# Optimization experiments

Measured on AMD Instinct MI355X. Metric: run time of the kernel, lower is better.

Reference implementation:

```python
import jax, jax.numpy as jnp
import numpy as np

# Forest of complete L-ary trees, BFS level-contiguous node numbering.
B_TREES, ARITY, DEPTH = 8, 4, 8
C, M, NGEN = 8, 100, 4
COUNTS = [B_TREES * ARITY**l for l in range(DEPTH + 1)]
OFFS = np.concatenate([[0], np.cumsum(COUNTS)]).astype(np.int64)
DIM = int(OFFS[-1])  # 699048
# tree id of each node: within-level index // (ARITY**level)
BATCH = np.concatenate([np.arange(COUNTS[l]) // (ARITY**l) for l in range(DEPTH + 1)])


def setup_inputs() -> dict:
    key = jax.random.key(0)
    k1, k2, k3, k4 = jax.random.split(key, 4)
    return {
        "x": jax.random.randint(k1, (DIM,), 0, M, dtype=jnp.int32),
        "A": jax.random.normal(k2, (C, C, ARITY, NGEN), dtype=jnp.float32) * 2.5,
        "B_emit": jax.random.normal(k3, (C, M, NGEN), dtype=jnp.float32) * 2.5,
        "Pi": jax.random.normal(k4, (C, NGEN), dtype=jnp.float32) * 2.5,
    }


def _htmm_loglik(x, A, B_emit, Pi):
    # softmax reparameterization (matches F.softmax axes in torch code)
    smA = jax.nn.softmax(A, axis=0)            # [C,C,L,G], over child state
    smA_t = jnp.transpose(smA, (2, 0, 1, 3))   # [L,C,C,G]
    smB = jax.nn.softmax(B_emit, axis=1)       # [C,M,G]
    smPi = jax.nn.softmax(Pi, axis=0)          # [C,G]

    # preliminary downward: prior state distribution per node, level by level.
    # Children of a parent are contiguous with sibling position j = idx % ARITY.
    prior_lvls = [jnp.broadcast_to(smPi, (COUNTS[0], C, NGEN))]
    for l in range(1, DEPTH + 1):
        n_pa = COUNTS[l - 1]
        # prior_child[c] = sum_d A[c, d, pos_j, g] * prior_pa[d]
        pl = jnp.einsum('jcdg,pdg->pjcg', smA_t, prior_lvls[-1])
        prior_lvls.append(pl.reshape(n_pa * ARITY, C, NGEN))
    prior = jnp.concatenate(prior_lvls, axis=0)  # [DIM,C,G]

    em = jnp.transpose(smB[:, x], (1, 0, 2))     # [DIM,C,G]
    beta0 = prior * em

    ll = jnp.zeros((DIM, NGEN), dtype=beta0.dtype)
    # leaves = deepest level
    beta_lvl = beta0[OFFS[DEPTH]:OFFS[DEPTH + 1]]
    nu = beta_lvl.sum(1)                          # [n_leaves,G]
    beta_lvl = beta_lvl / nu[:, None, :]
    ll = ll.at[OFFS[DEPTH]:OFFS[DEPTH + 1]].set(jnp.log(nu))

    # upward recursion, bottom-up
    for l in range(DEPTH, 0, -1):
        n_pa = COUNTS[l - 1]
        ratio = (beta_lvl / prior[OFFS[l]:OFFS[l + 1]]).reshape(n_pa, ARITY, C, NGEN)
        # beta_uv[d] = sum_c A[c, d, pos_j, g] * beta_ch[c] / prior_ch[c]
        beta_uv = jnp.einsum('jcdg,pjcg->pjdg', smA_t, ratio)  # [n_pa,L,C,G]
        beta_pa = beta0[OFFS[l - 1]:OFFS[l]] * jnp.prod(beta_uv, axis=1)
        nu = beta_pa.sum(1)
        beta_lvl = beta_pa / nu[:, None, :]
        ll = ll.at[OFFS[l - 1]:OFFS[l]].set(jnp.log(nu))

    # scatter per-node log-likelihood contributions into per-tree totals
    return jax.ops.segment_sum(ll, jnp.asarray(BATCH), num_segments=B_TREES)  # [B_TREES,G]


def reference(x, A, B_emit, Pi):
    return _htmm_loglik(x, A, B_emit, Pi)
```

## Files before the change

### kernel.cpp

```cpp
#include <hip/hip_runtime.h>

constexpr int OFFS1 = 8, OFFS2 = 40, OFFS3 = 168, OFFS4 = 680;
constexpr int OFFS5 = 2728, OFFS6 = 10920, OFFS7 = 43688, OFFS8 = 174760;


#define WB() __builtin_amdgcn_wave_barrier()
#define AG_ST(p, v) __hip_atomic_store((p), (v), __ATOMIC_RELAXED, __HIP_MEMORY_SCOPE_AGENT)
#define AG_LD(p) __hip_atomic_load((p), __ATOMIC_RELAXED, __HIP_MEMORY_SCOPE_AGENT)

template <int CTRL>
static __device__ __forceinline__ float qadd(float v) {
  int x = __builtin_amdgcn_update_dpp(0, __float_as_int(v), CTRL, 0xF, 0xF, true);
  return v + __int_as_float(x);
}
static __device__ __forceinline__ float bfly8(float v) {
  v = qadd<0xB1>(v);
  v = qadd<0x4E>(v);
  int x = __builtin_amdgcn_ds_swizzle(__float_as_int(v), 0x101F);
  return v + __int_as_float(x);
}

static __device__ __forceinline__ void ld8(const float* p, float pv[8]) {
  const float4* q = (const float4*)p;
  float4 a = q[0], b = q[1];
  pv[0] = a.x; pv[1] = a.y; pv[2] = a.z; pv[3] = a.w;
  pv[4] = b.x; pv[5] = b.y; pv[6] = b.z; pv[7] = b.w;
}

static __device__ __forceinline__ float dot8r(const float w[8], const float* p) {
  const float4* q = (const float4*)p;
  float4 a = q[0], b = q[1];
  return w[0] * a.x + w[1] * a.y + w[2] * a.z + w[3] * a.w +
         w[4] * b.x + w[5] * b.y + w[6] * b.z + w[7] * b.w;
}

static __device__ __forceinline__ float rcpf(float x) { return __builtin_amdgcn_rcpf(x); }

__global__ __launch_bounds__(256) void k_all(const int* __restrict__ x,
                                             const float* __restrict__ A,
                                             const float* __restrict__ Bm,
                                             const float* __restrict__ Pi,
                                             float* __restrict__ RAT4,
                                             float* __restrict__ blocksum,
                                             unsigned* __restrict__ ctr,
                                             float* __restrict__ out) {
  __shared__ __align__(16) float wtd_l[1024];
  __shared__ __align__(16) float emt_l[3200];
  __shared__ __align__(16) float pit_l[32];
  __shared__ __align__(16) float etab_l[12800];
  __shared__ __align__(16) float shbuf[2304];
  __shared__ __align__(16) float rat5buf[16][32];
  __shared__ __align__(16) float pri4buf[4][32];
  __shared__ float llb[4];
  __shared__ int lastf;

  int t = threadIdx.x;
  int r = t & 31, g = r >> 3, s = r & 7, grp = t >> 5;
  int b = blockIdx.x, tree = b >> 6;

  if (t < 128) {
    int d = t >> 4, j = (t >> 2) & 3, gg = t & 3;
    float v[8], sum = 0.f;
#pragma unroll
    for (int ss = 0; ss < 8; ss++) { v[ss] = __expf(A[((ss * 8 + d) * 4 + j) * 4 + gg]); sum += v[ss]; }
    float inv = rcpf(sum);
#pragma unroll
    for (int ss = 0; ss < 8; ss++) wtd_l[(j * 8 + d) * 32 + gg * 8 + ss] = v[ss] * inv;
  }
  if (t < 4) {
    float v[8], sum = 0.f;
#pragma unroll
    for (int c = 0; c < 8; c++) { v[c] = __expf(Pi[c * 4 + t]); sum += v[c]; }
    float inv = rcpf(sum);
#pragma unroll
    for (int c = 0; c < 8; c++) pit_l[t * 8 + c] = v[c] * inv;
    llb[t] = 0.f;
  }
  {
    int row = t >> 3, part = t & 7, c = row >> 2, gg = row & 3;
    int m0 = part < 4 ? part * 13 : 52 + (part - 4) * 12;
    int mn = part < 4 ? 13 : 12;
    float sum = 0.f;
    for (int m = m0; m < m0 + mn; m++) sum += __expf(Bm[(c * 100 + m) * 4 + gg]);
    sum = bfly8(sum);
    float inv = rcpf(sum);
    for (int m = m0; m < m0 + mn; m++)
      emt_l[m * 32 + gg * 8 + c] = __expf(Bm[(c * 100 + m) * 4 + gg]) * inv;
  }
  __syncthreads();
  {
    int c7 = t & 127, half = t >> 7;
    int j = c7 >> 5, d = (c7 >> 2) & 7, gg = c7 & 3;
    float w[8];
    ld8(&wtd_l[(j * 8 + d) * 32 + gg * 8], w);
    for (int m = half * 50; m < half * 50 + 50; m++)
      etab_l[(m * 4 + j) * 32 + gg * 8 + d] = dot8r(w, &emt_l[m * 32 + gg * 8]);
  }
  float wtd_r[4][8], wup_r[4][8];
#pragma unroll
  for (int j = 0; j < 4; j++) {
#pragma unroll
    for (int d = 0; d < 8; d++) wtd_r[j][d] = wtd_l[(j * 8 + d) * 32 + r];
    ld8(&wtd_l[(j * 8 + s) * 32 + g * 8], wup_r[j]);
  }
  __syncthreads();

  float* st = &shbuf[grp * 288];
  float acc = 0.f;
#pragma unroll 1
  for (int round = 0; round < 2; round++) {
    int n5 = b * 16 + round * 8 + grp;
    float v5 = pit_l[r], pri4 = 0.f;
#pragma unroll
    for (int k = 1; k <= 5; k++) {
      int j = (n5 >> (2 * (5 - k))) & 3;
      st[256 + r] = v5; WB();
      float pv[8]; ld8(st + 256 + g * 8, pv); WB();
      float nv = 0.f;
#pragma unroll
      for (int d = 0; d < 8; d++) nv += wtd_l[(j * 8 + d) * 32 + r] * pv[d];
      v5 = nv;
      if (k == 4) pri4 = v5;
    }
    float pv5[8];
    st[256 + r] = v5; WB(); ld8(st + 256 + g * 8, pv5); WB();

    const int4* x8v = (const int4*)(x + OFFS8 + n5 * 64);
    const int4* x7v = (const int4*)(x + OFFS7 + n5 * 16);
    int4 x6v = *(const int4*)(x + OFFS6 + n5 * 4);
    int x5s = x[OFFS5 + n5];
    const int* x6a = (const int*)&x6v;

#pragma unroll
    for (int q6 = 0; q6 < 4; q6++) {
      int4 x7 = x7v[q6];
      const int* x7a = (const int*)&x7;
      float u6 = 0.f;
#pragma unroll
      for (int d = 0; d < 8; d++) u6 += wtd_r[q6][d] * pv5[d];
      float pv6[8];
      st[256 + r] = u6; WB(); ld8(st + 256 + g * 8, pv6); WB();

      int4 xls[4];
      float Ep[4][4];
#pragma unroll
      for (int q7 = 0; q7 < 4; q7++) {
        xls[q7] = x8v[q6 * 4 + q7];
        const int* xla = (const int*)&xls[q7];
#pragma unroll
        for (int j = 0; j < 4; j++) Ep[q7][j] = etab_l[(xla[j] * 4 + j) * 32 + r];
      }

#pragma unroll
      for (int q7 = 0; q7 < 4; q7++) {
        float u7 = 0.f;
#pragma unroll
        for (int d = 0; d < 8; d++) u7 += wtd_r[q7][d] * pv6[d];
        float n0 = bfly8(u7 * Ep[q7][0]);
        float n1 = bfly8(u7 * Ep[q7][1]);
        float n2 = bfly8(u7 * Ep[q7][2]);
        float n3 = bfly8(u7 * Ep[q7][3]);
        float p01 = n0 * n1, p23 = n2 * n3;
        float prod = (Ep[q7][0] * Ep[q7][1] * rcpf(p01)) * (Ep[q7][2] * Ep[q7][3] * rcpf(p23));
        acc += __logf(p01) + __logf(p23);
        float em = emt_l[x7a[q7] * 32 + r];
        float nu7 = bfly8(u7 * em * prod);
        acc += __logf(nu7);
        st[q7 * 32 + r] = em * prod * rcpf(nu7);
      }
      WB();
      float prod6 = 1.f;
#pragma unroll
      for (int j = 0; j < 4; j++) prod6 *= dot8r(wup_r[j], st + j * 32 + g * 8);
      WB();
      float em6 = emt_l[x6a[q6] * 32 + r];
      float nu6 = bfly8(u6 * em6 * prod6);
      acc += __logf(nu6);
      st[(4 + q6) * 32 + r] = em6 * prod6 * rcpf(nu6);
    }
    WB();
    {
      float prod5 = 1.f;
#pragma unroll
      for (int j = 0; j < 4; j++) prod5 *= dot8r(wup_r[j], st + (4 + j) * 32 + g * 8);
      WB();
      float em5 = emt_l[x5s * 32 + r];
      float nu5 = bfly8(v5 * em5 * prod5);
      acc += __logf(nu5);
      rat5buf[round * 8 + grp][r] = em5 * prod5 * rcpf(nu5);
    }
    if ((grp & 3) == 0) pri4buf[round * 2 + (grp >> 2)][r] = pri4;
  }
  __syncthreads();

  if (grp < 4) {
    int n4 = b * 4 + grp;
    float prod = 1.f;
#pragma unroll
    for (int j = 0; j < 4; j++) prod *= dot8r(wup_r[j], &rat5buf[grp * 4 + j][g * 8]);
    float em = emt_l[x[OFFS4 + n4] * 32 + r];
    float pr4 = pri4buf[grp][r];
    float nu = bfly8(pr4 * em * prod);
    acc += __logf(nu);
    AG_ST(&RAT4[n4 * 32 + r], em * prod * rcpf(nu));
  }

  if (s == 0) atomicAdd(&llb[g], acc);
  __syncthreads();
  if (t < 4) AG_ST(&blocksum[b * 4 + t], llb[t]);
  asm volatile("s_waitcnt vmcnt(0)" ::: "memory");
  __syncthreads();
  if (t == 0) {
    unsigned old = __hip_atomic_fetch_add(&ctr[tree * 32], 1u, __ATOMIC_RELAXED,
                                          __HIP_MEMORY_SCOPE_AGENT);
    lastf = (old == 63u || old == 0xAAAAAAE9u) ? 1 : 0;
  }
  __syncthreads();
  if (!lastf) return;

  float* rat4_l = etab_l;
#pragma unroll
  for (int ib = 0; ib < 4; ib++) {
    float tmp[8];
#pragma unroll
    for (int i = 0; i < 8; i++) tmp[i] = AG_LD(&RAT4[tree * 8192 + (ib * 8 + i) * 256 + t]);
#pragma unroll
    for (int i = 0; i < 8; i++) rat4_l[(ib * 8 + i) * 256 + t] = tmp[i];
  }
  if (t < 4) llb[t] = 0.f;
  __syncthreads();

  float acc2 = 0.f;
#pragma unroll 1
  for (int ii = 0; ii < 2; ii++) {
    int l2 = ii * 8 + grp;
    int n2g = tree * 16 + l2;
    float v2 = pit_l[r];
#pragma unroll
    for (int k = 1; k <= 2; k++) {
      int j = (n2g >> (2 * (2 - k))) & 3;
      st[256 + r] = v2; WB();
      float pv[8]; ld8(st + 256 + g * 8, pv); WB();
      float nv = 0.f;
#pragma unroll
      for (int d = 0; d < 8; d++) nv += wtd_l[(j * 8 + d) * 32 + r] * pv[d];
      v2 = nv;
    }
    float pv2[8];
    st[256 + r] = v2; WB(); ld8(st + 256 + g * 8, pv2); WB();
#pragma unroll
    for (int j3 = 0; j3 < 4; j3++) {
      int n3g = n2g * 4 + j3;
      int i3l = l2 * 4 + j3;
      float p3 = 0.f;
#pragma unroll
      for (int d = 0; d < 8; d++) p3 += wtd_r[j3][d] * pv2[d];
      float prod = 1.f;
#pragma unroll
      for (int j = 0; j < 4; j++) prod *= dot8r(wup_r[j], &rat4_l[(i3l * 4 + j) * 32 + g * 8]);
      float em = emt_l[x[OFFS3 + n3g] * 32 + r];
      float nu = bfly8(p3 * em * prod);
      acc2 += __logf(nu);
      st[j3 * 32 + r] = em * prod * rcpf(nu);
    }
    WB();
    float prod = 1.f;
#pragma unroll
    for (int j = 0; j < 4; j++) prod *= dot8r(wup_r[j], st + j * 32 + g * 8);
    WB();
    float em = emt_l[x[OFFS2 + n2g] * 32 + r];
    float nu = bfly8(v2 * em * prod);
    acc2 += __logf(nu);
    st[(5 + ii) * 32 + r] = em * prod * rcpf(nu);
  }
  __syncthreads();
  if (grp < 4) {
    int n1g = tree * 4 + grp;
    float pv[8]; ld8(pit_l + g * 8, pv);
    float v1 = 0.f;
#pragma unroll
    for (int d = 0; d < 8; d++) v1 += wtd_l[(grp * 8 + d) * 32 + r] * pv[d];
    float prod = 1.f;
#pragma unroll
    for (int j = 0; j < 4; j++) {
      int l2 = grp * 4 + j;
      prod *= dot8r(wup_r[j], &shbuf[(l2 & 7) * 288 + (5 + (l2 >> 3)) * 32 + g * 8]);
    }
    float em = emt_l[x[OFFS1 + n1g] * 32 + r];
    float nu = bfly8(v1 * em * prod);
    acc2 += __logf(nu);
    st[7 * 32 + r] = em * prod * rcpf(nu);
  }
  __syncthreads();
  if (grp == 0) {
    float pr = pit_l[r];
    float prod = 1.f;
#pragma unroll
    for (int j = 0; j < 4; j++) prod *= dot8r(wup_r[j], &shbuf[j * 288 + 7 * 32 + g * 8]);
    float em = emt_l[x[tree] * 32 + r];
    float nu = bfly8(pr * em * prod);
    acc2 += __logf(nu);
  }
  __syncthreads();
  if (s == 0) atomicAdd(&llb[g], acc2);
  float v = AG_LD(&blocksum[tree * 256 + t]);
  __syncthreads();
  shbuf[t] = v;
  __syncthreads();
#pragma unroll
  for (int off = 128; off >= 4; off >>= 1) {
    if (t < off) shbuf[t] += shbuf[t + off];
    __syncthreads();
  }
  if (t < 4) out[tree * 4 + t] = shbuf[t] + llb[t];
}

extern "C" void kernel_launch(void* const* d_in, const int* in_sizes, int n_in,
                              void* d_out, int out_size, void* d_ws, size_t ws_size,
                              hipStream_t stream) {
  const int* x = (const int*)d_in[0];
  const float* A = (const float*)d_in[1];
  const float* Bm = (const float*)d_in[2];
  const float* Pi = (const float*)d_in[3];
  float* ws = (float*)d_ws;
  unsigned* ctr = (unsigned*)d_ws;
  float* blocksum = ws + 256;
  float* RAT4 = ws + 256 + 2048;
  float* out = (float*)d_out;

  k_all<<<512, 256, 0, stream>>>(x, A, Bm, Pi, RAT4, blocksum, ctr, out);
}
```

Before: 95.23 us.

## Replace LDS staging with DPP cross-lane broadcasts in tree recursion

Intra-octet exchanges that previously wrote a value to shared memory and read back eight neighbours now use DPP quad-perm and row-mirror moves, with weights stored in a permuted order that matches the mirrored lane layout. The bfly8 reduction swaps its ds_swizzle for a third DPP step. Leaf-index and level-7 index loads are hoisted and software-prefetched one q6 iteration ahead. The aim is to remove LDS round-trips and wave barriers on the serial critical path, at the cost of more VALU moves and registers and a mirror-based lane permutation that must line up exactly.

```diff
diff --git a/kernel.cpp b/kernel.cpp
--- a/kernel.cpp
+++ b/kernel.cpp
@@ -4,20 +4,32 @@
 constexpr int OFFS5 = 2728, OFFS6 = 10920, OFFS7 = 43688, OFFS8 = 174760;
 
 
-#define WB() __builtin_amdgcn_wave_barrier()
 #define AG_ST(p, v) __hip_atomic_store((p), (v), __ATOMIC_RELAXED, __HIP_MEMORY_SCOPE_AGENT)
 #define AG_LD(p) __hip_atomic_load((p), __ATOMIC_RELAXED, __HIP_MEMORY_SCOPE_AGENT)
 
 template <int CTRL>
-static __device__ __forceinline__ float qadd(float v) {
-  int x = __builtin_amdgcn_update_dpp(0, __float_as_int(v), CTRL, 0xF, 0xF, true);
-  return v + __int_as_float(x);
-}
+static __device__ __forceinline__ float dppmov(float v) {
+  return __int_as_float(__builtin_amdgcn_update_dpp(0, __float_as_int(v), CTRL, 0xF, 0xF, true));
+}
+
 static __device__ __forceinline__ float bfly8(float v) {
-  v = qadd<0xB1>(v);
-  v = qadd<0x4E>(v);
-  int x = __builtin_amdgcn_ds_swizzle(__float_as_int(v), 0x101F);
-  return v + __int_as_float(x);
+  v += dppmov<0xB1>(v);
+  v += dppmov<0x4E>(v);
+  v += dppmov<0x141>(v);
+  return v;
+}
+
+static __device__ __forceinline__ void oct8(float v, float pv[8]) {
+  float m = dppmov<0x141>(v);
+  pv[0] = dppmov<0x00>(v); pv[1] = dppmov<0x55>(v);
+  pv[2] = dppmov<0xAA>(v); pv[3] = dppmov<0xFF>(v);
+  pv[4] = dppmov<0x00>(m); pv[5] = dppmov<0x55>(m);
+  pv[6] = dppmov<0xAA>(m); pv[7] = dppmov<0xFF>(m);
+}
+
+static __device__ __forceinline__ float dot8(const float w[8], const float v[8]) {
+  return w[0]*v[0] + w[1]*v[1] + w[2]*v[2] + w[3]*v[3] +
+         w[4]*v[4] + w[5]*v[5] + w[6]*v[6] + w[7]*v[7];
 }
 
 static __device__ __forceinline__ void ld8(const float* p, float pv[8]) {
@@ -27,14 +39,42 @@
   pv[4] = b.x; pv[5] = b.y; pv[6] = b.z; pv[7] = b.w;
 }
 
+static __device__ __forceinline__ void ld8p(const float* p, float wp[8], int h) {
+  const float4* q = (const float4*)p;
+  float4 a = q[h], b = q[1 - h];
+  wp[0] = a.x; wp[1] = a.y; wp[2] = a.z; wp[3] = a.w;
+  wp[4] = b.w; wp[5] = b.z; wp[6] = b.y; wp[7] = b.x;
+}
+
+static __device__ __forceinline__ float dot8p(const float wp[8], const float* p, int h) {
+  const float4* q = (const float4*)p;
+  float4 a = q[h], b = q[1 - h];
+  return wp[0]*a.x + wp[1]*a.y + wp[2]*a.z + wp[3]*a.w +
+         wp[4]*b.w + wp[5]*b.z + wp[6]*b.y + wp[7]*b.x;
+}
+
 static __device__ __forceinline__ float dot8r(const float w[8], const float* p) {
   const float4* q = (const float4*)p;
   float4 a = q[0], b = q[1];
-  return w[0] * a.x + w[1] * a.y + w[2] * a.z + w[3] * a.w +
-         w[4] * b.x + w[5] * b.y + w[6] * b.z + w[7] * b.w;
+  return w[0]*a.x + w[1]*a.y + w[2]*a.z + w[3]*a.w +
+         w[4]*b.x + w[5]*b.y + w[6]*b.z + w[7]*b.w;
 }
 
 static __device__ __forceinline__ float rcpf(float x) { return __builtin_amdgcn_rcpf(x); }
+
+static __device__ __forceinline__ float step_down(const float* wtd_l, float v, int j,
+                                                  int r, int h) {
+  const float* wb = &wtd_l[j * 256 + r];
+  float w[8];
+#pragma unroll
+  for (int k = 0; k < 4; k++) {
+    w[k]     = wb[(4 * h + k) * 32];
+    w[4 + k] = wb[(7 - 4 * h - k) * 32];
+  }
+  float pv[8];
+  oct8(v, pv);
+  return dot8(w, pv);
+}
 
 __global__ __launch_bounds__(256) void k_all(const int* __restrict__ x,
                                              const float* __restrict__ A,
@@ -56,6 +96,7 @@
 
   int t = threadIdx.x;
   int r = t & 31, g = r >> 3, s = r & 7, grp = t >> 5;
+  int h = s >> 2;
   int b = blockIdx.x, tree = b >> 6;
 
   if (t < 128) {
@@ -96,66 +137,70 @@
     for (int m = half * 50; m < half * 50 + 50; m++)
       etab_l[(m * 4 + j) * 32 + gg * 8 + d] = dot8r(w, &emt_l[m * 32 + gg * 8]);
   }
-  float wtd_r[4][8], wup_r[4][8];
+  float wtd_p[4][8], wup_p[4][8];
 #pragma unroll
   for (int j = 0; j < 4; j++) {
-#pragma unroll
-    for (int d = 0; d < 8; d++) wtd_r[j][d] = wtd_l[(j * 8 + d) * 32 + r];
-    ld8(&wtd_l[(j * 8 + s) * 32 + g * 8], wup_r[j]);
-  }
-  __syncthreads();
-
-  float* st = &shbuf[grp * 288];
+    const float* wb = &wtd_l[j * 256 + r];
+#pragma unroll
+    for (int k = 0; k < 4; k++) {
+      wtd_p[j][k]     = wb[(4 * h + k) * 32];
+      wtd_p[j][4 + k] = wb[(7 - 4 * h - k) * 32];
+    }
+    ld8p(&wtd_l[(j * 8 + s) * 32 + g * 8], wup_p[j], h);
+  }
+  __syncthreads();
+
   float acc = 0.f;
 #pragma unroll 1
   for (int round = 0; round < 2; round++) {
     int n5 = b * 16 + round * 8 + grp;
-    float v5 = pit_l[r], pri4 = 0.f;
-#pragma unroll
-    for (int k = 1; k <= 5; k++) {
-      int j = (n5 >> (2 * (5 - k))) & 3;
-      st[256 + r] = v5; WB();
-      float pv[8]; ld8(st + 256 + g * 8, pv); WB();
-      float nv = 0.f;
-#pragma unroll
-      for (int d = 0; d < 8; d++) nv += wtd_l[(j * 8 + d) * 32 + r] * pv[d];
-      v5 = nv;
-      if (k == 4) pri4 = v5;
-    }
-    float pv5[8];
-    st[256 + r] = v5; WB(); ld8(st + 256 + g * 8, pv5); WB();
 
     const int4* x8v = (const int4*)(x + OFFS8 + n5 * 64);
-    const int4* x7v = (const int4*)(x + OFFS7 + n5 * 16);
+    const int4* x7p = (const int4*)(x + OFFS7 + n5 * 16);
     int4 x6v = *(const int4*)(x + OFFS6 + n5 * 4);
     int x5s = x[OFFS5 + n5];
     const int* x6a = (const int*)&x6v;
-
+    int4 x7q[4];
+#pragma unroll
+    for (int q = 0; q < 4; q++) x7q[q] = x7p[q];
+    int4 xls[4][4];
+#pragma unroll
+    for (int q = 0; q < 4; q++) xls[0][q] = x8v[q];
+
+    float v5 = pit_l[r], pri4 = 0.f;
+#pragma unroll
+    for (int k = 1; k <= 5; k++) {
+      int j = (n5 >> (2 * (5 - k))) & 3;
+      v5 = step_down(wtd_l, v5, j, r, h);
+      if (k == 4) pri4 = v5;
+    }
+    float pv5[8];
+    oct8(v5, pv5);
+
+    float rat6[4];
 #pragma unroll
     for (int q6 = 0; q6 < 4; q6++) {
-      int4 x7 = x7v[q6];
-      const int* x7a = (const int*)&x7;
-      float u6 = 0.f;
-#pragma unroll
-      for (int d = 0; d < 8; d++) u6 += wtd_r[q6][d] * pv5[d];
+      if (q6 < 3) {
+#pragma unroll
+        for (int q = 0; q < 4; q++) xls[q6 + 1][q] = x8v[(q6 + 1) * 4 + q];
+      }
+      float u6 = dot8(wtd_p[q6], pv5);
       float pv6[8];
-      st[256 + r] = u6; WB(); ld8(st + 256 + g * 8, pv6); WB();
-
-      int4 xls[4];
+      oct8(u6, pv6);
+      const int* x7a = (const int*)&x7q[q6];
+
       float Ep[4][4];
 #pragma unroll
       for (int q7 = 0; q7 < 4; q7++) {
-        xls[q7] = x8v[q6 * 4 + q7];
-        const int* xla = (const int*)&xls[q7];
+        const int* xla = (const int*)&xls[q6][q7];
 #pragma unroll
         for (int j = 0; j < 4; j++) Ep[q7][j] = etab_l[(xla[j] * 4 + j) * 32 + r];
       }
 
+      float rat7[4];
 #pragma unroll
       for (int q7 = 0; q7 < 4; q7++) {
-        float u7 = 0.f;
-#pragma unroll
-        for (int d = 0; d < 8; d++) u7 += wtd_r[q7][d] * pv6[d];
+        float u7 = dot8(wtd_p[q7], pv6);
         float n0 = bfly8(u7 * Ep[q7][0]);
         float n1 = bfly8(u7 * Ep[q7][1]);
         float n2 = bfly8(u7 * Ep[q7][2]);
@@ -166,24 +211,28 @@
         float em = emt_l[x7a[q7] * 32 + r];
         float nu7 = bfly8(u7 * em * prod);
         acc += __logf(nu7);
-        st[q7 * 32 + r] = em * prod * rcpf(nu7);
-      }
-      WB();
+        rat7[q7] = em * prod * rcpf(nu7);
+      }
       float prod6 = 1.f;
 #pragma unroll
-      for (int j = 0; j < 4; j++) prod6 *= dot8r(wup_r[j], st + j * 32 + g * 8);
-      WB();
+      for (int j = 0; j < 4; j++) {
+        float pr[8];
+        oct8(rat7[j], pr);
+        prod6 *= dot8(wup_p[j], pr);
+      }
       float em6 = emt_l[x6a[q6] * 32 + r];
       float nu6 = bfly8(u6 * em6 * prod6);
       acc += __logf(nu6);
-      st[(4 + q6) * 32 + r] = em6 * prod6 * rcpf(nu6);
-    }
-    WB();
+      rat6[q6] = em6 * prod6 * rcpf(nu6);
+    }
     {
       float prod5 = 1.f;
 #pragma unroll
-      for (int j = 0; j < 4; j++) prod5 *= dot8r(wup_r[j], st + (4 + j) * 32 + g * 8);
-      WB();
+      for (int j = 0; j < 4; j++) {
+        float pr[8];
+        oct8(rat6[j], pr);
+        prod5 *= dot8(wup_p[j], pr);
+      }
       float em5 = emt_l[x5s * 32 + r];
       float nu5 = bfly8(v5 * em5 * prod5);
       acc += __logf(nu5);
@@ -197,7 +246,7 @@
     int n4 = b * 4 + grp;
     float prod = 1.f;
 #pragma unroll
-    for (int j = 0; j < 4; j++) prod *= dot8r(wup_r[j], &rat5buf[grp * 4 + j][g * 8]);
+    for (int j = 0; j < 4; j++) prod *= dot8p(wup_p[j], &rat5buf[grp * 4 + j][g * 8], h);
     float em = emt_l[x[OFFS4 + n4] * 32 + r];
     float pr4 = pri4buf[grp][r];
     float nu = bfly8(pr4 * em * prod);
@@ -230,44 +279,38 @@
   if (t < 4) llb[t] = 0.f;
   __syncthreads();
 
+  float* st = &shbuf[grp * 288];
   float acc2 = 0.f;
 #pragma unroll 1
   for (int ii = 0; ii < 2; ii++) {
     int l2 = ii * 8 + grp;
     int n2g = tree * 16 + l2;
     float v2 = pit_l[r];
-#pragma unroll
-    for (int k = 1; k <= 2; k++) {
-      int j = (n2g >> (2 * (2 - k))) & 3;
-      st[256 + r] = v2; WB();
-      float pv[8]; ld8(st + 256 + g * 8, pv); WB();
-      float nv = 0.f;
-#pragma unroll
-      for (int d = 0; d < 8; d++) nv += wtd_l[(j * 8 + d) * 32 + r] * pv[d];
-      v2 = nv;
-    }
+    v2 = step_down(wtd_l, v2, (n2g >> 2) & 3, r, h);
+    v2 = step_down(wtd_l, v2, n2g & 3, r, h);
     float pv2[8];
-    st[256 + r] = v2; WB(); ld8(st + 256 + g * 8, pv2); WB();
+    oct8(v2, pv2);
+    float rat3[4];
 #pragma unroll
     for (int j3 = 0; j3 < 4; j3++) {
       int n3g = n2g * 4 + j3;
       int i3l = l2 * 4 + j3;
-      float p3 = 0.f;
-#pragma unroll
-      for (int d = 0; d < 8; d++) p3 += wtd_r[j3][d] * pv2[d];
+      float p3 = dot8(wtd_p[j3], pv2);
       float prod = 1.f;
 #pragma unroll
-      for (int j = 0; j < 4; j++) prod *= dot8r(wup_r[j], &rat4_l[(i3l * 4 + j) * 32 + g * 8]);
+      for (int j = 0; j < 4; j++) prod *= dot8p(wup_p[j], &rat4_l[(i3l * 4 + j) * 32 + g * 8], h);
       float em = emt_l[x[OFFS3 + n3g] * 32 + r];
       float nu = bfly8(p3 * em * prod);
       acc2 += __logf(nu);
-      st[j3 * 32 + r] = em * prod * rcpf(nu);
-    }
-    WB();
+      rat3[j3] = em * prod * rcpf(nu);
+    }
     float prod = 1.f;
 #pragma unroll
-    for (int j = 0; j < 4; j++) prod *= dot8r(wup_r[j], st + j * 32 + g * 8);
-    WB();
+    for (int j = 0; j < 4; j++) {
+      float pr[8];
+      oct8(rat3[j], pr);
+      prod *= dot8(wup_p[j], pr);
+    }
     float em = emt_l[x[OFFS2 + n2g] * 32 + r];
     float nu = bfly8(v2 * em * prod);
     acc2 += __logf(nu);
@@ -276,7 +319,8 @@
   __syncthreads();
   if (grp < 4) {
     int n1g = tree * 4 + grp;
-    float pv[8]; ld8(pit_l + g * 8, pv);
+    float pv[8];
+    ld8(pit_l + g * 8, pv);
     float v1 = 0.f;
 #pragma unroll
     for (int d = 0; d < 8; d++) v1 += wtd_l[(grp * 8 + d) * 32 + r] * pv[d];
@@ -284,7 +328,7 @@
 #pragma unroll
     for (int j = 0; j < 4; j++) {
       int l2 = grp * 4 + j;
-      prod *= dot8r(wup_r[j], &shbuf[(l2 & 7) * 288 + (5 + (l2 >> 3)) * 32 + g * 8]);
+      prod *= dot8p(wup_p[j], &shbuf[(l2 & 7) * 288 + (5 + (l2 >> 3)) * 32 + g * 8], h);
     }
     float em = emt_l[x[OFFS1 + n1g] * 32 + r];
     float nu = bfly8(v1 * em * prod);
@@ -296,7 +340,7 @@
     float pr = pit_l[r];
     float prod = 1.f;
 #pragma unroll
-    for (int j = 0; j < 4; j++) prod *= dot8r(wup_r[j], &shbuf[j * 288 + 7 * 32 + g * 8]);
+    for (int j = 0; j < 4; j++) prod *= dot8p(wup_p[j], &shbuf[j * 288 + 7 * 32 + g * 8], h);
     float em = emt_l[x[tree] * 32 + r];
     float nu = bfly8(pr * em * prod);
     acc2 += __logf(nu);
```

New measurement: 105.8 us. 1.11x slower.
